# Kernel tuning notes

Hardware: AMD Instinct MI355X
Metric: run time of the kernel (lower is better)

## Reference

```python
import jax, jax.numpy as jnp
import numpy as np

N = 50000          # nodes
E = 1600000        # edges
H = 8              # heads
F = 16             # out feats per head (np1class)
IN = 256           # in feats
NEG_SLOPE = 0.2    # DGL GATConv default leaky_relu slope


def setup_inputs() -> dict:
    key = jax.random.key(0)
    ks = jax.random.split(key, 7)
    x = jax.random.normal(ks[0], (N, IN), dtype=jnp.float32)
    W = jax.random.normal(ks[1], (IN, H * F), dtype=jnp.float32) * 0.05
    attn_l = jax.random.normal(ks[2], (H, F), dtype=jnp.float32) * 0.05
    attn_r = jax.random.normal(ks[3], (H, F), dtype=jnp.float32) * 0.05
    bias = jax.random.normal(ks[4], (H * F,), dtype=jnp.float32) * 0.05
    src = jax.random.randint(ks[5], (E,), 0, N, dtype=jnp.int64)
    dst = jax.random.randint(ks[6], (E,), 0, N, dtype=jnp.int64)
    return {"x": x, "W": W, "attn_l": attn_l, "attn_r": attn_r,
            "bias": bias, "src": src, "dst": dst}


def reference(x, W, attn_l, attn_r, bias, src, dst):
    # Linear projection to heads: [N, H, F]
    feat = (x @ W).reshape(N, H, F)
    # Per-node attention halves: [N, H]
    el = jnp.einsum('nhf,hf->nh', feat, attn_l)
    er = jnp.einsum('nhf,hf->nh', feat, attn_r)
    # Edge scores: e = leaky_relu(el[src] + er[dst])  -> [E, H]
    e = jax.nn.leaky_relu(el[src] + er[dst], negative_slope=NEG_SLOPE)
    # Segment softmax over incoming edges of each destination node
    m = jax.ops.segment_max(e, dst, num_segments=N)           # [N, H]
    m = jnp.where(jnp.isfinite(m), m, 0.0)                    # empty segments
    m = jax.lax.stop_gradient(m)
    ex = jnp.exp(e - m[dst])                                  # [E, H]
    s = jax.ops.segment_sum(ex, dst, num_segments=N)          # [N, H]
    a = ex / jnp.maximum(s[dst], 1e-9)                        # [E, H]
    # Weighted aggregation of source features: [N, H, F]
    msg = a[:, :, None] * feat[src]
    rst = jax.ops.segment_sum(msg, dst, num_segments=N)
    rst = rst + bias.reshape(H, F)
    # Classifier: mean over heads -> [N, F]
    return rst.mean(axis=1)
```

## Files before the change

### kernel.cpp

```cpp
#include <hip/hip_runtime.h>
#include <hip/hip_bf16.h>

#define NH 8
#define NF 16
#define NIN 256
#define HF 128
#define CAP 3072
#define BCH 4096

typedef __attribute__((ext_vector_type(8))) short bf16x8;
typedef __attribute__((ext_vector_type(4))) float f32x4;

__device__ __forceinline__ unsigned short f2bf(float f) {
    union { float f; unsigned int u; } v; v.f = f;
    unsigned int r = v.u + 0x7FFFu + ((v.u >> 16) & 1u);
    return (unsigned short)(r >> 16);
}
__device__ __forceinline__ float bf2f(unsigned short b) {
    union { unsigned int u; float f; } v; v.u = ((unsigned int)b) << 16;
    return v.f;
}

#define GROWS 128
__global__ __launch_bounds__(256) void gemm_mfma(const float* __restrict__ A,
                                                 const float* __restrict__ W,
                                                 const float* __restrict__ attn_l,
                                                 const float* __restrict__ attn_r,
                                                 unsigned short* __restrict__ featb,
                                                 float* __restrict__ el,
                                                 float* __restrict__ er, int M) {
    __shared__ unsigned short AsH[32][264];
    __shared__ unsigned short AsL[32][264];
    const int tid = threadIdx.x;
    const int wave = tid >> 6, lane = tid & 63;
    const int quad = lane >> 4, lq = lane & 15;
    const int row0 = blockIdx.x * GROWS;

    bf16x8 bfrag[8][2];
#pragma unroll
    for (int h2 = 0; h2 < 2; h2++) {
        const int col = (wave * 2 + h2) * 16 + lq;
#pragma unroll
        for (int kk = 0; kk < 8; kk++) {
            const int kb = kk * 32 + quad * 8;
            bf16x8 f;
#pragma unroll
            for (int j = 0; j < 8; j++)
                f[j] = (short)f2bf(W[(size_t)(kb + j) * HF + col]);
            bfrag[kk][h2] = f;
        }
    }
    const float al0 = attn_l[(wave * 2 + 0) * 16 + lq];
    const float al1 = attn_l[(wave * 2 + 1) * 16 + lq];
    const float ar0 = attn_r[(wave * 2 + 0) * 16 + lq];
    const float ar1 = attn_r[(wave * 2 + 1) * 16 + lq];

    const int srow = tid >> 3;

    for (int c = 0; c < 4; c++) {
        const int crow0 = row0 + c * 32;
        __syncthreads();
#pragma unroll
        for (int i = 0; i < 8; i++) {
            const int col = ((tid & 7) + i * 8) * 4;
            const int gr = crow0 + srow;
            float4 v = make_float4(0.f, 0.f, 0.f, 0.f);
            if (gr < M) v = *(const float4*)&A[(size_t)gr * NIN + col];
            const unsigned short h0 = f2bf(v.x), h1 = f2bf(v.y),
                                 h2b = f2bf(v.z), h3 = f2bf(v.w);
            *(ushort4*)&AsH[srow][col] = make_ushort4(h0, h1, h2b, h3);
            *(ushort4*)&AsL[srow][col] =
                make_ushort4(f2bf(v.x - bf2f(h0)), f2bf(v.y - bf2f(h1)),
                             f2bf(v.z - bf2f(h2b)), f2bf(v.w - bf2f(h3)));
        }
        __syncthreads();
#pragma unroll
        for (int s = 0; s < 2; s++) {
            f32x4 acc0 = {0.f, 0.f, 0.f, 0.f};
            f32x4 acc1 = {0.f, 0.f, 0.f, 0.f};
            const int ar = s * 16 + lq;
#pragma unroll
            for (int kk = 0; kk < 8; kk++) {
                const bf16x8 ah = *(const bf16x8*)&AsH[ar][kk * 32 + quad * 8];
                const bf16x8 al = *(const bf16x8*)&AsL[ar][kk * 32 + quad * 8];
                acc0 = __builtin_amdgcn_mfma_f32_16x16x32_bf16(ah, bfrag[kk][0], acc0, 0, 0, 0);
                acc1 = __builtin_amdgcn_mfma_f32_16x16x32_bf16(ah, bfrag[kk][1], acc1, 0, 0, 0);
                acc0 = __builtin_amdgcn_mfma_f32_16x16x32_bf16(al, bfrag[kk][0], acc0, 0, 0, 0);
                acc1 = __builtin_amdgcn_mfma_f32_16x16x32_bf16(al, bfrag[kk][1], acc1, 0, 0, 0);
            }
#pragma unroll
            for (int r = 0; r < 4; r++) {
                const int gr = crow0 + s * 16 + quad * 4 + r;
                float pl0 = acc0[r] * al0, pr0 = acc0[r] * ar0;
                float pl1 = acc1[r] * al1, pr1 = acc1[r] * ar1;
#pragma unroll
                for (int m = 1; m < 16; m <<= 1) {
                    pl0 += __shfl_xor(pl0, m, 64);
                    pr0 += __shfl_xor(pr0, m, 64);
                    pl1 += __shfl_xor(pl1, m, 64);
                    pr1 += __shfl_xor(pr1, m, 64);
                }
                if (gr < M) {
                    featb[(size_t)gr * HF + (wave * 2 + 0) * 16 + lq] = f2bf(acc0[r]);
                    featb[(size_t)gr * HF + (wave * 2 + 1) * 16 + lq] = f2bf(acc1[r]);
                    if (lq == 0) {
                        el[(size_t)gr * NH + wave * 2 + 0] = pl0;
                        el[(size_t)gr * NH + wave * 2 + 1] = pl1;
                        er[(size_t)gr * NH + wave * 2 + 0] = pr0;
                        er[(size_t)gr * NH + wave * 2 + 1] = pr1;
                    }
                }
            }
        }
    }
}

__global__ __launch_bounds__(256) void bin_kernel(const int* __restrict__ src,
                                                  const int* __restrict__ dst,
                                                  unsigned int* __restrict__ binned,
                                                  unsigned int* __restrict__ runtab,
                                                  int E, int NB) {
    __shared__ unsigned int hist[784];
    __shared__ unsigned int offs[784];
    __shared__ unsigned short lpos[BCH];
    __shared__ unsigned int obuf[BCH];
    __shared__ int dcache[BCH];
    __shared__ unsigned int wsum[4];
    __shared__ unsigned int sbase;
    const int blk = blockIdx.x, t = threadIdx.x;
    const int base = blk * BCH;
    const int cnt = min(BCH, E - base);
    const int lane = t & 63, w = t >> 6;
    for (int b = t; b < NB; b += 256) hist[b] = 0;
    for (int i = t; i < cnt; i += 256) dcache[i] = dst[base + i];
    if (t == 0) sbase = 0;
    __syncthreads();
    for (int i = t; i < cnt; i += 256)
        lpos[i] = (unsigned short)atomicAdd(&hist[dcache[i] >> 6], 1u);
    __syncthreads();
    for (int c0 = 0; c0 < NB; c0 += 256) {
        const int idx = c0 + t;
        const unsigned int v = (idx < NB) ? hist[idx] : 0;
        unsigned int incl = v;
#pragma unroll
        for (int off = 1; off < 64; off <<= 1) {
            const unsigned int x = __shfl_up(incl, off, 64);
            if (lane >= off) incl += x;
        }
        if (lane == 63) wsum[w] = incl;
        __syncthreads();
        unsigned int wbase = 0;
        for (int k = 0; k < w; k++) wbase += wsum[k];
        const unsigned int tot = wsum[0] + wsum[1] + wsum[2] + wsum[3];
        const unsigned int excl = sbase + wbase + incl - v;
        if (idx < NB) {
            offs[idx] = excl;
            runtab[(size_t)blk * NB + idx] = excl | (v << 16);
        }
        __syncthreads();
        if (t == 0) sbase += tot;
        __syncthreads();
    }
    for (int i = t; i < cnt; i += 256) {
        const int d = dcache[i];
        obuf[offs[d >> 6] + lpos[i]] =
            (unsigned int)src[base + i] | ((unsigned int)(d & 63) << 16);
    }
    __syncthreads();
    for (int i = t; i < cnt; i += 256) binned[(size_t)base + i] = obuf[i];
}

__global__ __launch_bounds__(256) void csr_kernel(const unsigned int* __restrict__ binned,
                                                  const unsigned int* __restrict__ runtab,
                                                  int* __restrict__ nodeinfo,
                                                  unsigned short* __restrict__ srcsw,
                                                  int N, int NB, int nbb) {
    __shared__ unsigned int eary[CAP];
    __shared__ unsigned short sSrc[CAP];
    __shared__ unsigned short roff[512];
    __shared__ unsigned short rcntl[512];
    __shared__ int rbase[512];
    __shared__ int len[64], cur[64];
    __shared__ unsigned int wsum[4];
    __shared__ unsigned int sbase;
    const int b = blockIdx.x, t = threadIdx.x;
    const int node0 = b << 6;
    const int lane = t & 63, w = t >> 6;
    if (t == 0) sbase = 0;
    __syncthreads();
    for (int c0 = 0; c0 < nbb; c0 += 256) {
        const int r = c0 + t;
        const unsigned int e = (r < nbb) ? runtab[(size_t)r * NB + b] : 0;
        const unsigned int v = e >> 16;
        unsigned int incl = v;
#pragma unroll
        for (int off = 1; off < 64; off <<= 1) {
            const unsigned int x = __shfl_up(incl, off, 64);
            if (lane >= off) incl += x;
        }
        if (lane == 63) wsum[w] = incl;
        __syncthreads();
        unsigned int wbase = 0;
        for (int k = 0; k < w; k++) wbase += wsum[k];
        const unsigned int tot = wsum[0] + wsum[1] + wsum[2] + wsum[3];
        if (r < nbb) {
            roff[r] = (unsigned short)(e & 0xFFFFu);
            rcntl[r] = (unsigned short)v;
            rbase[r] = (int)(sbase + wbase + incl - v);
        }
        __syncthreads();
        if (t == 0) sbase += tot;
        __syncthreads();
    }
    const int tot = (int)sbase;
    for (int r = t; r < nbb; r += 256) {
        const int off = (int)roff[r];
        const int pb = rbase[r];
        const int rc = (int)rcntl[r];
        const unsigned int* bp = &binned[(size_t)r * BCH + off];
        for (int j = 0; j < rc; j++) eary[pb + j] = bp[j];
    }
    if (t < 64) len[t] = 0;
    __syncthreads();
    for (int i = t; i < tot; i += 256) atomicAdd(&len[eary[i] >> 16], 1);
    __syncthreads();
    if (t < 64) {
        const int v = len[t];
        int incl = v;
#pragma unroll
        for (int off = 1; off < 64; off <<= 1) {
            const int x = __shfl_up(incl, off, 64);
            if (t >= off) incl += x;
        }
        const int excl = incl - v;
        cur[t] = excl;
        if (node0 + t < N) nodeinfo[node0 + t] = excl | (v << 16);
    }
    __syncthreads();
    for (int i = t; i < tot; i += 256) {
        const unsigned int p = eary[i];
        const int pos = atomicAdd(&cur[p >> 16], 1);
        sSrc[pos] = (unsigned short)(p & 0xFFFFu);
    }
    __syncthreads();
    unsigned short* sw = &srcsw[(size_t)b * CAP];
    for (int i = t; i < tot; i += 256) sw[i] = sSrc[i];
}

__global__ __launch_bounds__(128) void agg_kernel(const int* __restrict__ nodeinfo,
                                                  const unsigned short* __restrict__ srcsw,
                                                  const float* __restrict__ el,
                                                  const float* __restrict__ er,
                                                  const unsigned short* __restrict__ featb,
                                                  const float* __restrict__ bias,
                                                  float* __restrict__ out) {
    const int n = blockIdx.x;
    const int tid = threadIdx.x;
    __shared__ float lds_sc[32][8];
    __shared__ int lds_src[32];
    __shared__ float lds_ps[128];
    __shared__ float lds_s[8];
    __shared__ float2 lds_acc[2][64];
    __shared__ float2 lds_v[8][8];

    const int info = nodeinfo[n];
    const int begin = (n >> 6) * CAP + (info & 0xFFFF);
    const int end = begin + (info >> 16);
    const int hA = tid & 7, eA = tid >> 3;
    const float er_h = er[(size_t)n * NH + hA];
    const int w = tid >> 6, lane = tid & 63;
    const int hB = lane >> 3, fB2 = lane & 7;

    float2 acc = make_float2(0.f, 0.f);
    float psum = 0.f;
    for (int base = begin; base < end; base += 32) {
        const int cn = min(32, end - base);
#pragma unroll
        for (int rep = 0; rep < 2; rep++) {
            const int ei = eA + rep * 16;
            if (ei < cn) {
                const int si = (int)srcsw[base + ei];
                if (hA == 0) lds_src[ei] = si;
                float v = el[(size_t)si * NH + hA] + er_h;
                v = v > 0.f ? v : 0.2f * v;
                const float sc = __expf(v);
                lds_sc[ei][hA] = sc;
                psum += sc;
            }
        }
        __syncthreads();
        unsigned int fv[16];
#pragma unroll
        for (int j = 0; j < 16; j++) {
            const int ej = w * 16 + j;
            const int sj = lds_src[ej];
            fv[j] = (ej < cn)
                        ? *(const unsigned int*)&featb[(size_t)sj * HF + hB * 16 + fB2 * 2]
                        : 0u;
        }
#pragma unroll
        for (int j = 0; j < 16; j++) {
            const int ej = w * 16 + j;
            const float sc = (ej < cn) ? lds_sc[ej][hB] : 0.f;
            acc.x = fmaf(sc, bf2f((unsigned short)(fv[j] & 0xFFFFu)), acc.x);
            acc.y = fmaf(sc, bf2f((unsigned short)(fv[j] >> 16)), acc.y);
        }
        __syncthreads();
    }

    lds_ps[tid] = psum;
    lds_acc[w][lane] = acc;
    __syncthreads();
    if (tid < 8) {
        float s = 0.f;
#pragma unroll
        for (int k = 0; k < 16; k++) s += lds_ps[k * 8 + tid];
        lds_s[tid] = fmaxf(s, 1e-9f);
    }
    __syncthreads();
    if (tid < 64) {
        const float2 t0 = lds_acc[0][tid], t1 = lds_acc[1][tid];
        const float inv = 1.f / lds_s[hB];
        float2 val;
        val.x = (t0.x + t1.x) * inv + bias[hB * 16 + fB2 * 2];
        val.y = (t0.y + t1.y) * inv + bias[hB * 16 + fB2 * 2 + 1];
        lds_v[hB][fB2] = val;
    }
    __syncthreads();
    if (tid < 8) {
        float2 o = make_float2(0.f, 0.f);
#pragma unroll
        for (int h = 0; h < 8; h++) {
            const float2 v = lds_v[h][tid];
            o.x += v.x; o.y += v.y;
        }
        o.x *= 0.125f; o.y *= 0.125f;
        *(float2*)&out[(size_t)n * 16 + tid * 2] = o;
    }
}

extern "C" void kernel_launch(void* const* d_in, const int* in_sizes, int n_in,
                              void* d_out, int out_size, void* d_ws, size_t ws_size,
                              hipStream_t stream) {
    const float* x      = (const float*)d_in[0];
    const float* W      = (const float*)d_in[1];
    const float* attn_l = (const float*)d_in[2];
    const float* attn_r = (const float*)d_in[3];
    const float* bias   = (const float*)d_in[4];
    const int*   src    = (const int*)d_in[5];
    const int*   dst    = (const int*)d_in[6];
    float* out = (float*)d_out;

    const int N = in_sizes[0] / NIN;
    const int E = in_sizes[5];
    const int NB = (N + 63) >> 6;
    const int nbb = (E + BCH - 1) / BCH;

    char* w = (char*)d_ws;
    unsigned short* featb = (unsigned short*)w; w += (size_t)N * HF * 2;
    float* el     = (float*)w; w += (size_t)N * NH * 4;
    float* er     = (float*)w; w += (size_t)N * NH * 4;
    int* nodeinfo = (int*)w;   w += (size_t)N * 4;
    unsigned int* binned = (unsigned int*)w; w += (size_t)nbb * BCH * 4;
    unsigned int* runtab = (unsigned int*)w; w += (size_t)nbb * NB * 4;
    unsigned short* srcsw = (unsigned short*)w;

    gemm_mfma<<<(N + GROWS - 1) / GROWS, 256, 0, stream>>>(x, W, attn_l, attn_r,
                                                           featb, el, er, N);
    bin_kernel<<<nbb, 256, 0, stream>>>(src, dst, binned, runtab, E, NB);
    csr_kernel<<<NB, 256, 0, stream>>>(binned, runtab, nodeinfo, srcsw, N, NB, nbb);
    agg_kernel<<<N, 128, 0, stream>>>(nodeinfo, srcsw, el, er, featb, bias, out);
}
```

Before: 229.2 us.

## Widen agg feature gathers to 16-byte loads with packed FMA and transpose runtab

The aggregation kernel now handles 64 edges per round instead of 32. Each lane gathers a 16-byte chunk (8 bf16 features) per edge instead of 4 bytes, so one wave covers four edges per load, and the weighted sums use v_pk_fma_f32 with a shuffle-xor reduction across edge slots. The bin run table is transposed so that csr_kernel reads it contiguously rather than with stride NB. Together these target gather transaction count and uncoalesced table reads, in exchange for more registers for the uint4 buffers and a reworked epilogue.

```diff
diff --git a/kernel.cpp b/kernel.cpp
--- a/kernel.cpp
+++ b/kernel.cpp
@@ -10,6 +10,7 @@
 
 typedef __attribute__((ext_vector_type(8))) short bf16x8;
 typedef __attribute__((ext_vector_type(4))) float f32x4;
+typedef __attribute__((ext_vector_type(2))) float f32x2;
 
 __device__ __forceinline__ unsigned short f2bf(float f) {
     union { float f; unsigned int u; } v; v.f = f;
@@ -128,6 +129,7 @@
     __shared__ unsigned int wsum[4];
     __shared__ unsigned int sbase;
     const int blk = blockIdx.x, t = threadIdx.x;
+    const int nbb = gridDim.x;
     const int base = blk * BCH;
     const int cnt = min(BCH, E - base);
     const int lane = t & 63, w = t >> 6;
@@ -155,7 +157,7 @@
         const unsigned int excl = sbase + wbase + incl - v;
         if (idx < NB) {
             offs[idx] = excl;
-            runtab[(size_t)blk * NB + idx] = excl | (v << 16);
+            runtab[(size_t)idx * nbb + blk] = excl | (v << 16);
         }
         __syncthreads();
         if (t == 0) sbase += tot;
@@ -190,7 +192,7 @@
     __syncthreads();
     for (int c0 = 0; c0 < nbb; c0 += 256) {
         const int r = c0 + t;
-        const unsigned int e = (r < nbb) ? runtab[(size_t)r * NB + b] : 0;
+        const unsigned int e = (r < nbb) ? runtab[(size_t)b * nbb + r] : 0;
         const unsigned int v = e >> 16;
         unsigned int incl = v;
 #pragma unroll
@@ -247,6 +249,7 @@
     for (int i = t; i < tot; i += 256) sw[i] = sSrc[i];
 }
 
+#define RND 64
 __global__ __launch_bounds__(128) void agg_kernel(const int* __restrict__ nodeinfo,
                                                   const unsigned short* __restrict__ srcsw,
                                                   const float* __restrict__ el,
@@ -256,12 +259,11 @@
                                                   float* __restrict__ out) {
     const int n = blockIdx.x;
     const int tid = threadIdx.x;
-    __shared__ float lds_sc[32][8];
-    __shared__ int lds_src[32];
+    __shared__ float lds_sc[RND][8];
+    __shared__ int   lds_src[RND];
     __shared__ float lds_ps[128];
-    __shared__ float lds_s[8];
-    __shared__ float2 lds_acc[2][64];
-    __shared__ float2 lds_v[8][8];
+    __shared__ float lds_r[2][16][9];
+    __shared__ float lds_o[16][9];
 
     const int info = nodeinfo[n];
     const int begin = (n >> 6) * CAP + (info & 0xFFFF);
@@ -269,14 +271,17 @@
     const int hA = tid & 7, eA = tid >> 3;
     const float er_h = er[(size_t)n * NH + hA];
     const int w = tid >> 6, lane = tid & 63;
-    const int hB = lane >> 3, fB2 = lane & 7;
-
-    float2 acc = make_float2(0.f, 0.f);
+    const int e4 = lane >> 4, p = lane & 15;
+    const int hB = p >> 1;
+    const int w4 = w * 4;
+
+    f32x2 acc0 = {0.f, 0.f}, acc1 = {0.f, 0.f}, acc2 = {0.f, 0.f}, acc3 = {0.f, 0.f};
     float psum = 0.f;
-    for (int base = begin; base < end; base += 32) {
-        const int cn = min(32, end - base);
-#pragma unroll
-        for (int rep = 0; rep < 2; rep++) {
+
+    for (int base = begin; base < end; base += RND) {
+        const int cn = min(RND, end - base);
+#pragma unroll
+        for (int rep = 0; rep < 4; rep++) {
             const int ei = eA + rep * 16;
             if (ei < cn) {
                 const int si = (int)srcsw[base + ei];
@@ -289,53 +294,72 @@
             }
         }
         __syncthreads();
-        unsigned int fv[16];
-#pragma unroll
-        for (int j = 0; j < 16; j++) {
-            const int ej = w * 16 + j;
-            const int sj = lds_src[ej];
-            fv[j] = (ej < cn)
-                        ? *(const unsigned int*)&featb[(size_t)sj * HF + hB * 16 + fB2 * 2]
-                        : 0u;
-        }
-#pragma unroll
-        for (int j = 0; j < 16; j++) {
-            const int ej = w * 16 + j;
-            const float sc = (ej < cn) ? lds_sc[ej][hB] : 0.f;
-            acc.x = fmaf(sc, bf2f((unsigned short)(fv[j] & 0xFFFFu)), acc.x);
-            acc.y = fmaf(sc, bf2f((unsigned short)(fv[j] >> 16)), acc.y);
-        }
-        __syncthreads();
-    }
-
+        const int jmax = __builtin_amdgcn_readfirstlane(
+            cn > w4 ? ((cn - w4 + 7) >> 3) : 0);
+        uint4 fv[8];
+#pragma unroll
+        for (int j = 0; j < 8; j++) {
+            if (j < jmax) {
+                const int ej = j * 8 + w4 + e4;
+                if (ej < cn)
+                    fv[j] = *(const uint4*)&featb[(size_t)lds_src[ej] * HF + p * 8];
+                else
+                    fv[j] = make_uint4(0u, 0u, 0u, 0u);
+            }
+        }
+#pragma unroll
+        for (int j = 0; j < 8; j++) {
+            if (j < jmax) {
+                const int ej = j * 8 + w4 + e4;
+                const float sc = (ej < cn) ? lds_sc[ej][hB] : 0.f;
+                const f32x2 sc2 = {sc, sc};
+                const unsigned int d0 = fv[j].x, d1 = fv[j].y,
+                                   d2 = fv[j].z, d3 = fv[j].w;
+                f32x2 v0, v1, v2, v3;
+                v0.x = __uint_as_float(d0 << 16); v0.y = __uint_as_float(d0 & 0xffff0000u);
+                v1.x = __uint_as_float(d1 << 16); v1.y = __uint_as_float(d1 & 0xffff0000u);
+                v2.x = __uint_as_float(d2 << 16); v2.y = __uint_as_float(d2 & 0xffff0000u);
+                v3.x = __uint_as_float(d3 << 16); v3.y = __uint_as_float(d3 & 0xffff0000u);
+                asm("v_pk_fma_f32 %0, %1, %2, %0" : "+v"(acc0) : "v"(v0), "v"(sc2));
+                asm("v_pk_fma_f32 %0, %1, %2, %0" : "+v"(acc1) : "v"(v1), "v"(sc2));
+                asm("v_pk_fma_f32 %0, %1, %2, %0" : "+v"(acc2) : "v"(v2), "v"(sc2));
+                asm("v_pk_fma_f32 %0, %1, %2, %0" : "+v"(acc3) : "v"(v3), "v"(sc2));
+            }
+        }
+        __syncthreads();
+    }
+
+#pragma unroll
+    for (int m = 16; m < 64; m <<= 1) {
+        acc0.x += __shfl_xor(acc0.x, m, 64); acc0.y += __shfl_xor(acc0.y, m, 64);
+        acc1.x += __shfl_xor(acc1.x, m, 64); acc1.y += __shfl_xor(acc1.y, m, 64);
+        acc2.x += __shfl_xor(acc2.x, m, 64); acc2.y += __shfl_xor(acc2.y, m, 64);
+        acc3.x += __shfl_xor(acc3.x, m, 64); acc3.y += __shfl_xor(acc3.y, m, 64);
+    }
     lds_ps[tid] = psum;
-    lds_acc[w][lane] = acc;
-    __syncthreads();
-    if (tid < 8) {
+    if (lane < 16) {
+        float* r = lds_r[w][lane];
+        r[0] = acc0.x; r[1] = acc0.y; r[2] = acc1.x; r[3] = acc1.y;
+        r[4] = acc2.x; r[5] = acc2.y; r[6] = acc3.x; r[7] = acc3.y;
+    }
+    __syncthreads();
+    if (tid < 16) {
+        const int h = tid >> 1;
         float s = 0.f;
 #pragma unroll
-        for (int k = 0; k < 16; k++) s += lds_ps[k * 8 + tid];
-        lds_s[tid] = fmaxf(s, 1e-9f);
-    }
-    __syncthreads();
-    if (tid < 64) {
-        const float2 t0 = lds_acc[0][tid], t1 = lds_acc[1][tid];
-        const float inv = 1.f / lds_s[hB];
-        float2 val;
-        val.x = (t0.x + t1.x) * inv + bias[hB * 16 + fB2 * 2];
-        val.y = (t0.y + t1.y) * inv + bias[hB * 16 + fB2 * 2 + 1];
-        lds_v[hB][fB2] = val;
-    }
-    __syncthreads();
-    if (tid < 8) {
-        float2 o = make_float2(0.f, 0.f);
-#pragma unroll
-        for (int h = 0; h < 8; h++) {
-            const float2 v = lds_v[h][tid];
-            o.x += v.x; o.y += v.y;
-        }
-        o.x *= 0.125f; o.y *= 0.125f;
-        *(float2*)&out[(size_t)n * 16 + tid * 2] = o;
+        for (int k = 0; k < 16; k++) s += lds_ps[k * 8 + h];
+        const float inv = 1.f / fmaxf(s, 1e-9f);
+#pragma unroll
+        for (int k = 0; k < 8; k++)
+            lds_o[tid][k] = (lds_r[0][tid][k] + lds_r[1][tid][k]) * inv;
+    }
+    __syncthreads();
+    if (tid < 16) {
+        float o = 0.f;
+#pragma unroll
+        for (int h = 0; h < 8; h++)
+            o += lds_o[h * 2 + (tid >> 3)][tid & 7] + bias[h * 16 + tid];
+        out[(size_t)n * 16 + tid] = o * 0.125f;
     }
 }
 
```

New measurement: 265.1 us. 1.16x slower.

## Process one destination node per wavefront in aggregation kernel

Applied to the files above, without the earlier changes.

The aggregation kernel switches from one 128-thread block per node to one 64-lane wavefront per node, four nodes per 256-thread block. Block-wide __syncthreads and the LDS-based reductions are replaced by wave barriers and cross-lane shuffles, and the edge window grows to 64. This removes block synchronization overhead and cuts the launch to a quarter as many blocks. The risk is load imbalance between nodes that share a block and less memory-level parallelism per node, since a single wave now gathers all of a node's source features.

```diff
diff --git a/kernel.cpp b/kernel.cpp
--- a/kernel.cpp
+++ b/kernel.cpp
@@ -247,95 +247,87 @@
     for (int i = t; i < tot; i += 256) sw[i] = sSrc[i];
 }
 
-__global__ __launch_bounds__(128) void agg_kernel(const int* __restrict__ nodeinfo,
+#define WIN 64
+__global__ __launch_bounds__(256) void agg_kernel(const int* __restrict__ nodeinfo,
                                                   const unsigned short* __restrict__ srcsw,
                                                   const float* __restrict__ el,
                                                   const float* __restrict__ er,
                                                   const unsigned short* __restrict__ featb,
                                                   const float* __restrict__ bias,
-                                                  float* __restrict__ out) {
-    const int n = blockIdx.x;
+                                                  float* __restrict__ out, int N) {
+    __shared__ float lds_sc[4][WIN][8];
+    __shared__ int lds_src[4][WIN];
     const int tid = threadIdx.x;
-    __shared__ float lds_sc[32][8];
-    __shared__ int lds_src[32];
-    __shared__ float lds_ps[128];
-    __shared__ float lds_s[8];
-    __shared__ float2 lds_acc[2][64];
-    __shared__ float2 lds_v[8][8];
+    const int w = tid >> 6, lane = tid & 63;
+    const int n = blockIdx.x * 4 + w;
+    if (n >= N) return;
 
     const int info = nodeinfo[n];
     const int begin = (n >> 6) * CAP + (info & 0xFFFF);
     const int end = begin + (info >> 16);
-    const int hA = tid & 7, eA = tid >> 3;
+    const int hA = lane & 7, eA = lane >> 3;
     const float er_h = er[(size_t)n * NH + hA];
-    const int w = tid >> 6, lane = tid & 63;
     const int hB = lane >> 3, fB2 = lane & 7;
 
     float2 acc = make_float2(0.f, 0.f);
     float psum = 0.f;
-    for (int base = begin; base < end; base += 32) {
-        const int cn = min(32, end - base);
-#pragma unroll
-        for (int rep = 0; rep < 2; rep++) {
-            const int ei = eA + rep * 16;
+    for (int base = begin; base < end; base += WIN) {
+        const int cn = min(WIN, end - base);
+        __builtin_amdgcn_wave_barrier();
+#pragma unroll
+        for (int rep = 0; rep < 8; rep++) {
+            const int ei = rep * 8 + eA;
             if (ei < cn) {
                 const int si = (int)srcsw[base + ei];
-                if (hA == 0) lds_src[ei] = si;
+                if (hA == 0) lds_src[w][ei] = si;
                 float v = el[(size_t)si * NH + hA] + er_h;
                 v = v > 0.f ? v : 0.2f * v;
                 const float sc = __expf(v);
-                lds_sc[ei][hA] = sc;
+                lds_sc[w][ei][hA] = sc;
                 psum += sc;
             }
         }
-        __syncthreads();
-        unsigned int fv[16];
-#pragma unroll
-        for (int j = 0; j < 16; j++) {
-            const int ej = w * 16 + j;
-            const int sj = lds_src[ej];
-            fv[j] = (ej < cn)
-                        ? *(const unsigned int*)&featb[(size_t)sj * HF + hB * 16 + fB2 * 2]
-                        : 0u;
-        }
-#pragma unroll
-        for (int j = 0; j < 16; j++) {
-            const int ej = w * 16 + j;
-            const float sc = (ej < cn) ? lds_sc[ej][hB] : 0.f;
-            acc.x = fmaf(sc, bf2f((unsigned short)(fv[j] & 0xFFFFu)), acc.x);
-            acc.y = fmaf(sc, bf2f((unsigned short)(fv[j] >> 16)), acc.y);
-        }
-        __syncthreads();
-    }
-
-    lds_ps[tid] = psum;
-    lds_acc[w][lane] = acc;
-    __syncthreads();
-    if (tid < 8) {
-        float s = 0.f;
-#pragma unroll
-        for (int k = 0; k < 16; k++) s += lds_ps[k * 8 + tid];
-        lds_s[tid] = fmaxf(s, 1e-9f);
-    }
-    __syncthreads();
-    if (tid < 64) {
-        const float2 t0 = lds_acc[0][tid], t1 = lds_acc[1][tid];
-        const float inv = 1.f / lds_s[hB];
-        float2 val;
-        val.x = (t0.x + t1.x) * inv + bias[hB * 16 + fB2 * 2];
-        val.y = (t0.y + t1.y) * inv + bias[hB * 16 + fB2 * 2 + 1];
-        lds_v[hB][fB2] = val;
-    }
-    __syncthreads();
-    if (tid < 8) {
-        float2 o = make_float2(0.f, 0.f);
-#pragma unroll
-        for (int h = 0; h < 8; h++) {
-            const float2 v = lds_v[h][tid];
-            o.x += v.x; o.y += v.y;
-        }
-        o.x *= 0.125f; o.y *= 0.125f;
-        *(float2*)&out[(size_t)n * 16 + tid * 2] = o;
+        __builtin_amdgcn_wave_barrier();
+        for (int b0 = 0; b0 < cn; b0 += 16) {
+            unsigned int fv[16];
+#pragma unroll
+            for (int j = 0; j < 16; j++) {
+                const int ej = b0 + j;
+                const int sj = lds_src[w][ej];
+                fv[j] = (ej < cn)
+                            ? *(const unsigned int*)&featb[(size_t)sj * HF + hB * 16 + fB2 * 2]
+                            : 0u;
+            }
+#pragma unroll
+            for (int j = 0; j < 16; j++) {
+                const int ej = b0 + j;
+                const float sc = (ej < cn) ? lds_sc[w][ej][hB] : 0.f;
+                acc.x = fmaf(sc, bf2f((unsigned short)(fv[j] & 0xFFFFu)), acc.x);
+                acc.y = fmaf(sc, bf2f((unsigned short)(fv[j] >> 16)), acc.y);
+            }
+        }
+    }
+
+    float s = psum;
+    s += __shfl_xor(s, 8, 64);
+    s += __shfl_xor(s, 16, 64);
+    s += __shfl_xor(s, 32, 64);
+    const float s_h = __shfl(s, hB, 64);
+    const float inv = 1.f / fmaxf(s_h, 1e-9f);
+    float2 val;
+    val.x = acc.x * inv + bias[hB * 16 + fB2 * 2];
+    val.y = acc.y * inv + bias[hB * 16 + fB2 * 2 + 1];
+    val.x += __shfl_xor(val.x, 8, 64);
+    val.x += __shfl_xor(val.x, 16, 64);
+    val.x += __shfl_xor(val.x, 32, 64);
+    val.y += __shfl_xor(val.y, 8, 64);
+    val.y += __shfl_xor(val.y, 16, 64);
+    val.y += __shfl_xor(val.y, 32, 64);
+    if (lane < 8) {
+        float2 o;
+        o.x = val.x * 0.125f;
+        o.y = val.y * 0.125f;
+        *(float2*)&out[(size_t)n * 16 + lane * 2] = o;
     }
 }
 
@@ -369,5 +361,6 @@
                                                            featb, el, er, N);
     bin_kernel<<<nbb, 256, 0, stream>>>(src, dst, binned, runtab, E, NB);
     csr_kernel<<<NB, 256, 0, stream>>>(binned, runtab, nodeinfo, srcsw, N, NB, nbb);
-    agg_kernel<<<N, 128, 0, stream>>>(nodeinfo, srcsw, el, er, featb, bias, out);
-}
+    agg_kernel<<<(N + 3) / 4, 256, 0, stream>>>(nodeinfo, srcsw, el, er, featb, bias,
+                                                out, N);
+}
```

Result: no change. 228.6 us (-0.3%).
